# Kernel tuning notes

Measured on AMD Instinct MI355X. Metric: run time of the kernel, lower is better.

The kernel has to match this reference:

```python
import jax, jax.numpy as jnp
import numpy as np

T = 5          # Newton-Schulz iterations
EPS = 1e-5
NC = 64        # num_channels per group

def setup_inputs() -> dict:
    key = jax.random.key(0)
    X = jax.random.normal(key, (128, 256, 32, 32), dtype=jnp.float32)
    weight = jnp.ones((1, 256, 1, 1), dtype=jnp.float32)
    bias = jnp.zeros((1, 256, 1, 1), dtype=jnp.float32)
    return {"X": X, "weight": weight, "bias": bias}

def _iternorm(X):
    B, C, H, W = X.shape
    g = C // NC
    # [B,C,H,W] -> [C,B,H,W] -> [g, nc, m]
    x = jnp.transpose(X, (1, 0, 2, 3)).reshape(g, NC, -1)
    m = x.shape[-1]
    mean = x.mean(-1, keepdims=True)
    xc = x - mean                                   # [g, nc, m]
    I = jnp.eye(NC, dtype=X.dtype)
    Sigma = EPS * I + jnp.einsum('gdm,gem->gde', xc, xc) / m
    # rTr = 1 / trace(Sigma) per group
    rTr = 1.0 / jnp.trace(Sigma, axis1=1, axis2=2)[:, None, None]
    Sn = Sigma * rTr                                # normalized covariance
    P = jnp.broadcast_to(I, (g, NC, NC))
    for _ in range(T):
        P3 = jnp.matmul(jnp.matmul(P, P), P)
        P = 1.5 * P - 0.5 * jnp.matmul(P3, Sn)
    wm = P * jnp.sqrt(rTr)                          # whitening matrix [g,nc,nc]
    xn = jnp.matmul(wm, xc)                         # [g, nc, m]
    Xn = jnp.transpose(xn.reshape(C, B, H, W), (1, 0, 2, 3))
    return Xn

def reference(X, weight, bias):
    Xn = _iternorm(X)
    return Xn * weight + bias
```

## Files before the change

### kernel.cpp

```cpp
#include <hip/hip_runtime.h>
#include <hip/hip_bf16.h>
#include <cstddef>
#include <cstdint>

typedef __attribute__((ext_vector_type(8))) short s16x8;
typedef __attribute__((ext_vector_type(4))) float f32x4;

namespace {
constexpr int NB   = 128;
constexpr int NCH  = 256;
constexpr int SPA  = 1024;
constexpr int NCC  = 64;
constexpr int MT   = NB * SPA;
constexpr float EPSV = 1e-5f;
}

__device__ inline unsigned short f2bf(float f) {
    union { float f; unsigned u; } v; v.f = f;
    unsigned r = v.u + 0x7fffu + ((v.u >> 16) & 1u);
    return (unsigned short)(r >> 16);
}

__device__ inline s16x8 cvt8(float4 a, float4 b) {
    union { __hip_bfloat162 h[4]; s16x8 s; } u;
    u.h[0] = __float22bfloat162_rn(make_float2(a.x, a.y));
    u.h[1] = __float22bfloat162_rn(make_float2(a.z, a.w));
    u.h[2] = __float22bfloat162_rn(make_float2(b.x, b.y));
    u.h[3] = __float22bfloat162_rn(make_float2(b.z, b.w));
    return u.s;
}

__device__ inline s16x8 pack8(const float* v) {
    union { __hip_bfloat162 h[4]; s16x8 s; } u;
    u.h[0] = __float22bfloat162_rn(make_float2(v[0], v[1]));
    u.h[1] = __float22bfloat162_rn(make_float2(v[2], v[3]));
    u.h[2] = __float22bfloat162_rn(make_float2(v[4], v[5]));
    u.h[3] = __float22bfloat162_rn(make_float2(v[6], v[7]));
    return u.s;
}

__device__ inline void issue8(const float* const base[4], int ks, float4 r[4][2]) {
#pragma unroll
    for (int cb = 0; cb < 4; ++cb) {
        r[cb][0] = *reinterpret_cast<const float4*>(base[cb] + ks * 32);
        r[cb][1] = *reinterpret_cast<const float4*>(base[cb] + ks * 32 + 4);
    }
}
__device__ inline void finish8(const float4 r[4][2], s16x8 frag[4], float csum[4]) {
#pragma unroll
    for (int cb = 0; cb < 4; ++cb) {
        const float4 f0 = r[cb][0], f1 = r[cb][1];
        csum[cb] += (f0.x + f0.y) + (f0.z + f0.w) + (f1.x + f1.y) + (f1.z + f1.w);
        frag[cb] = cvt8(f0, f1);
    }
}
__device__ inline void mfma10(const s16x8 frag[4], f32x4 acc[10]) {
    int n = 0;
#pragma unroll
    for (int i = 0; i < 4; ++i)
#pragma unroll
        for (int j = i; j < 4; ++j) {
            acc[n] = __builtin_amdgcn_mfma_f32_16x16x32_bf16(frag[i], frag[j], acc[n], 0, 0, 0);
            ++n;
        }
}

__global__ __launch_bounds__(256) void zca_stats(const float* __restrict__ X,
                                                 float* __restrict__ Gpart,
                                                 float* __restrict__ Spart) {
    const int bid = blockIdx.x;
    const int g = bid >> 7, b = bid & 127;
    const int t = threadIdx.x;
    const int w = t >> 6, l = t & 63;
    const int lr = l & 15, gq = l >> 4;

    const float* xs = X + ((size_t)b * NCH + (size_t)g * NCC) * SPA;

    const float* base[4];
#pragma unroll
    for (int cb = 0; cb < 4; ++cb)
        base[cb] = xs + (size_t)(cb * 16 + lr) * SPA + w * 256 + gq * 8;

    f32x4 acc[10];
#pragma unroll
    for (int n = 0; n < 10; ++n) acc[n] = (f32x4){0.f, 0.f, 0.f, 0.f};
    float csum[4] = {0.f, 0.f, 0.f, 0.f};

    float4 rA[4][2], rB[4][2];
    issue8(base, 0, rA);
    issue8(base, 1, rB);
#pragma unroll
    for (int ks = 0; ks < 8; ks += 2) {
        s16x8 frag[4];
        finish8(rA, frag, csum);
        if (ks + 2 < 8) issue8(base, ks + 2, rA);
        mfma10(frag, acc);
        finish8(rB, frag, csum);
        if (ks + 3 < 8) issue8(base, ks + 3, rB);
        mfma10(frag, acc);
    }

    __shared__ float Gl[64 * 67];
    __shared__ float Ssl[4][64];

#pragma unroll
    for (int cb = 0; cb < 4; ++cb) {
        float s = csum[cb];
        s += __shfl_xor(s, 16, 64);
        s += __shfl_xor(s, 32, 64);
        if (gq == 0) Ssl[w][cb * 16 + lr] = s;
    }

    for (int ph = 0; ph < 4; ++ph) {
        if (w == ph) {
            int n = 0;
#pragma unroll
            for (int i = 0; i < 4; ++i)
#pragma unroll
                for (int j = i; j < 4; ++j) {
#pragma unroll
                    for (int q = 0; q < 4; ++q) {
                        const int d = i * 16 + gq * 4 + q;
                        const int e = j * 16 + lr;
                        const float val = acc[n][q];
                        if (ph == 0) {
                            Gl[d * 67 + e] = val;
                            if (i != j) Gl[e * 67 + d] = val;
                        } else {
                            Gl[d * 67 + e] += val;
                            if (i != j) Gl[e * 67 + d] += val;
                        }
                    }
                    ++n;
                }
        }
        __syncthreads();
    }

#pragma unroll
    for (int i = 0; i < 16; ++i) {
        const int idx = i * 256 + t;
        const int d = idx >> 6, e = idx & 63;
        Gpart[(size_t)bid * 4096 + idx] = Gl[d * 67 + e];
    }
    if (t < 64)
        Spart[(size_t)bid * 64 + t] =
            ((Ssl[0][t] + Ssl[1][t]) + (Ssl[2][t] + Ssl[3][t]));
}

__global__ __launch_bounds__(256) void zca_reduce(const float* __restrict__ Gpart,
                                                  const float* __restrict__ Spart,
                                                  float* __restrict__ Gsum,
                                                  float* __restrict__ Ssub) {
    const int g = blockIdx.x >> 4, eb = blockIdx.x & 15;
    const int t = threadIdx.x;
    const float* p = Gpart + (size_t)g * 128 * 4096 + eb * 256 + t;
    float a0 = 0.f, a1 = 0.f, a2 = 0.f, a3 = 0.f;
    for (int q = 0; q < 128; q += 4) {
        a0 += p[(size_t)(q + 0) * 4096];
        a1 += p[(size_t)(q + 1) * 4096];
        a2 += p[(size_t)(q + 2) * 4096];
        a3 += p[(size_t)(q + 3) * 4096];
    }
    Gsum[(size_t)g * 4096 + eb * 256 + t] = (a0 + a1) + (a2 + a3);

    if (t < 64) {
        float s = 0.f;
        for (int q = 0; q < 8; ++q)
            s += Spart[(size_t)(g * 128 + eb * 8 + q) * 64 + t];
        Ssub[(size_t)(g * 16 + eb) * 64 + t] = s;
    }
}

__global__ __launch_bounds__(256) void zca_newton(const float* __restrict__ Gsum,
                                                  const float* __restrict__ Ssub,
                                                  const float* __restrict__ weight,
                                                  const float* __restrict__ bias,
                                                  short* __restrict__ wmB,
                                                  float* __restrict__ betaOut) {
    const int g = blockIdx.x;
    const int t = threadIdx.x;
    const int v = t >> 4;
    const int u = t & 15;

    __shared__ float Pm[64 * 65];
    __shared__ float Sn[64 * 65];
    __shared__ float Ta[64 * 65];
    __shared__ float meanS[64];
    __shared__ float scal[2];

    if (t < 64) {
        float s = 0.f;
        for (int eb = 0; eb < 16; ++eb) s += Ssub[(size_t)(g * 16 + eb) * 64 + t];
        meanS[t] = s * (1.0f / MT);
    }
    __syncthreads();

#pragma unroll
    for (int i = 0; i < 16; ++i) {
        int idx = i * 256 + t;
        int d = idx >> 6, e = idx & 63;
        float sig = Gsum[(size_t)g * 4096 + idx] * (1.0f / MT)
                    - meanS[d] * meanS[e] + (d == e ? EPSV : 0.f);
        Sn[d * 65 + e] = sig;
    }
    __syncthreads();

    if (t < 64) {
        float tr = Sn[t * 65 + t];
        for (int off = 32; off > 0; off >>= 1) tr += __shfl_down(tr, off, 64);
        if (t == 0) {
            scal[0] = 1.0f / tr;
            scal[1] = sqrtf(1.0f / tr);
        }
    }
    __syncthreads();
    const float rTr = scal[0];

#pragma unroll
    for (int i = 0; i < 16; ++i) {
        int idx = i * 256 + t;
        int d = idx >> 6, e = idx & 63;
        Sn[d * 65 + e] *= rTr;
        Pm[d * 65 + e] = (d == e) ? 1.f : 0.f;
    }
    __syncthreads();

    auto mm = [&](const float* A, const float* Bm, float* r) {
#pragma unroll
        for (int q = 0; q < 16; ++q) r[q] = 0.f;
        for (int k = 0; k < 64; ++k) {
            float a[4], bb[4];
#pragma unroll
            for (int i = 0; i < 4; ++i) a[i] = A[(v + 16 * i) * 65 + k];
#pragma unroll
            for (int j = 0; j < 4; ++j) bb[j] = Bm[k * 65 + (u + 16 * j)];
#pragma unroll
            for (int i = 0; i < 4; ++i)
#pragma unroll
                for (int j = 0; j < 4; ++j) r[i * 4 + j] += a[i] * bb[j];
        }
    };
    auto storeTa = [&](const float* r) {
#pragma unroll
        for (int q = 0; q < 16; ++q)
            Ta[(v + 16 * (q >> 2)) * 65 + (u + 16 * (q & 3))] = r[q];
    };

    for (int it = 0; it < 5; ++it) {
        float r[16];
        mm(Pm, Sn, r);
        storeTa(r);
        __syncthreads();
        mm(Pm, Ta, r);
        __syncthreads();
        storeTa(r);
        __syncthreads();
        mm(Pm, Ta, r);
        __syncthreads();
#pragma unroll
        for (int q = 0; q < 16; ++q) {
            int rr = v + 16 * (q >> 2);
            int cc = u + 16 * (q & 3);
            Pm[rr * 65 + cc] = 1.5f * Pm[rr * 65 + cc] - 0.5f * r[q];
        }
        __syncthreads();
    }

    const float srTr = scal[1];
#pragma unroll
    for (int i = 0; i < 16; ++i) {
        int idx = i * 256 + t;
        int d = idx >> 6, e = idx & 63;
        float wv = weight[g * NCC + d];
        wmB[(size_t)g * 4096 + d * 64 + e] = (short)f2bf(Pm[d * 65 + e] * srTr * wv);
    }
    if (t < 64) {
        int d = t;
        float s = 0.f;
        for (int e = 0; e < 64; ++e) s += Pm[d * 65 + e] * meanS[e];
        betaOut[g * NCC + d] = bias[g * NCC + d] - weight[g * NCC + d] * srTr * s;
    }
}

__global__ __launch_bounds__(256) void zca_apply(const float* __restrict__ X,
                                                 const short* __restrict__ wmB,
                                                 const float* __restrict__ beta,
                                                 float* __restrict__ out) {
    const int bid = blockIdx.x;
    const int g  = bid & 3;
    const int qm = (bid >> 2) & 3;
    const int b  = bid >> 4;
    const int t  = threadIdx.x;
    const int w  = t >> 6, l = t & 63;
    const int lr = l & 15, gq = l >> 4;

    __shared__ float Xt[64][64];
    __shared__ float Ot[64][64];

    s16x8 wa[4][2];
#pragma unroll
    for (int i = 0; i < 4; ++i)
#pragma unroll
        for (int kc = 0; kc < 2; ++kc)
            wa[i][kc] = *reinterpret_cast<const s16x8*>(
                wmB + (size_t)g * 4096 + (16 * i + lr) * 64 + kc * 32 + gq * 8);

    const int ch = t >> 4, s4 = t & 15;
    float bst[4];
#pragma unroll
    for (int i = 0; i < 4; ++i) bst[i] = beta[g * NCC + i * 16 + ch];

    const float* xb = X + ((size_t)b * NCH + (size_t)g * NCC) * SPA + qm * 256;
    float* ob = out + ((size_t)b * NCH + (size_t)g * NCC) * SPA + qm * 256;

    const int lh = l >> 4;

    for (int tile = 0; tile < 4; ++tile) {
#pragma unroll
        for (int i = 0; i < 4; ++i) {
            const float* gsrc = xb + (size_t)(i * 16 + w * 4 + lh) * SPA
                                + tile * 64 + (l & 15) * 4;
            __builtin_amdgcn_global_load_lds(
                (const __attribute__((address_space(1))) void*)gsrc,
                (__attribute__((address_space(3))) void*)&Xt[i * 16 + w * 4][0],
                16, 0, 0);
        }
        asm volatile("s_waitcnt vmcnt(0)" ::: "memory");
        __syncthreads();

        float v[2][8];
#pragma unroll
        for (int kc = 0; kc < 2; ++kc)
#pragma unroll
            for (int j = 0; j < 8; ++j)
                v[kc][j] = Xt[kc * 32 + gq * 8 + j][w * 16 + lr];

        s16x8 bf0 = pack8(v[0]);
        s16x8 bf1 = pack8(v[1]);

        f32x4 acc[4];
#pragma unroll
        for (int i = 0; i < 4; ++i) acc[i] = (f32x4){0.f, 0.f, 0.f, 0.f};
#pragma unroll
        for (int i = 0; i < 4; ++i) {
            acc[i] = __builtin_amdgcn_mfma_f32_16x16x32_bf16(wa[i][0], bf0, acc[i], 0, 0, 0);
            acc[i] = __builtin_amdgcn_mfma_f32_16x16x32_bf16(wa[i][1], bf1, acc[i], 0, 0, 0);
        }

#pragma unroll
        for (int i = 0; i < 4; ++i)
#pragma unroll
            for (int q = 0; q < 4; ++q)
                Ot[16 * i + 4 * gq + q][w * 16 + lr] = acc[i][q];
        __syncthreads();

#pragma unroll
        for (int i = 0; i < 4; ++i) {
            float4 o = *reinterpret_cast<const float4*>(&Ot[i * 16 + ch][s4 * 4]);
            o.x += bst[i]; o.y += bst[i]; o.z += bst[i]; o.w += bst[i];
            *reinterpret_cast<float4*>(
                ob + (size_t)(i * 16 + ch) * SPA + tile * 64 + s4 * 4) = o;
        }
    }
}

extern "C" void kernel_launch(void* const* d_in, const int* in_sizes, int n_in,
                              void* d_out, int out_size, void* d_ws, size_t ws_size,
                              hipStream_t stream) {
    const float* X      = (const float*)d_in[0];
    const float* weight = (const float*)d_in[1];
    const float* bias   = (const float*)d_in[2];
    float* out = (float*)d_out;

    float* ws    = (float*)d_ws;
    float* Gpart = ws;
    float* Spart = Gpart + (size_t)512 * 4096;
    float* Gsum  = Spart + (size_t)512 * 64;
    float* Ssub  = Gsum + (size_t)4 * 4096;
    float* betaW = Ssub + (size_t)4 * 16 * 64;
    short* wmB   = (short*)(betaW + 256);

    zca_stats <<<dim3(512),  dim3(256), 0, stream>>>(X, Gpart, Spart);
    zca_reduce<<<dim3(64),   dim3(256), 0, stream>>>(Gpart, Spart, Gsum, Ssub);
    zca_newton<<<dim3(4),    dim3(256), 0, stream>>>(Gsum, Ssub, weight, bias, wmB, betaW);
    zca_apply <<<dim3(2048), dim3(256), 0, stream>>>(X, wmB, betaW, out);
}
```

Baseline: 138.8 us.

## Split zca_stats blocks in half along spatial dim to double grid parallelism

Each stats block now handles half of a (group, batch) spatial extent, so the grid doubles from 512 to 1024 blocks and each wave does 4 k-steps instead of 8. The load pipeline is reorganised into two half-channel register sets per step. The goal is better occupancy and latency hiding across the CUs for this bandwidth-bound Gram pass. In exchange, the partial-Gram workspace doubles, and zca_reduce must sum 256 partials per group instead of 128, which adds memory traffic in that small kernel.

```diff
diff --git a/kernel.cpp b/kernel.cpp
--- a/kernel.cpp
+++ b/kernel.cpp
@@ -39,19 +39,20 @@
     return u.s;
 }
 
-__device__ inline void issue8(const float* const base[4], int ks, float4 r[4][2]) {
-#pragma unroll
-    for (int cb = 0; cb < 4; ++cb) {
-        r[cb][0] = *reinterpret_cast<const float4*>(base[cb] + ks * 32);
-        r[cb][1] = *reinterpret_cast<const float4*>(base[cb] + ks * 32 + 4);
-    }
-}
-__device__ inline void finish8(const float4 r[4][2], s16x8 frag[4], float csum[4]) {
-#pragma unroll
-    for (int cb = 0; cb < 4; ++cb) {
-        const float4 f0 = r[cb][0], f1 = r[cb][1];
-        csum[cb] += (f0.x + f0.y) + (f0.z + f0.w) + (f1.x + f1.y) + (f1.z + f1.w);
-        frag[cb] = cvt8(f0, f1);
+__device__ inline void issue4(const float* const base[4], int ks, int p, float4 r[2][2]) {
+#pragma unroll
+    for (int c = 0; c < 2; ++c) {
+        const float* q = base[p * 2 + c] + ks * 32;
+        r[c][0] = *reinterpret_cast<const float4*>(q);
+        r[c][1] = *reinterpret_cast<const float4*>(q + 4);
+    }
+}
+__device__ inline void finish4(const float4 r[2][2], s16x8* frag2, float* cs2) {
+#pragma unroll
+    for (int c = 0; c < 2; ++c) {
+        const float4 f0 = r[c][0], f1 = r[c][1];
+        cs2[c] += (f0.x + f0.y) + (f0.z + f0.w) + (f1.x + f1.y) + (f1.z + f1.w);
+        frag2[c] = cvt8(f0, f1);
     }
 }
 __device__ inline void mfma10(const s16x8 frag[4], f32x4 acc[10]) {
@@ -69,7 +70,7 @@
                                                  float* __restrict__ Gpart,
                                                  float* __restrict__ Spart) {
     const int bid = blockIdx.x;
-    const int g = bid >> 7, b = bid & 127;
+    const int g = bid >> 8, b = (bid >> 1) & 127, half = bid & 1;
     const int t = threadIdx.x;
     const int w = t >> 6, l = t & 63;
     const int lr = l & 15, gq = l >> 4;
@@ -79,24 +80,23 @@
     const float* base[4];
 #pragma unroll
     for (int cb = 0; cb < 4; ++cb)
-        base[cb] = xs + (size_t)(cb * 16 + lr) * SPA + w * 256 + gq * 8;
+        base[cb] = xs + (size_t)(cb * 16 + lr) * SPA + half * 512 + w * 128 + gq * 8;
 
     f32x4 acc[10];
 #pragma unroll
     for (int n = 0; n < 10; ++n) acc[n] = (f32x4){0.f, 0.f, 0.f, 0.f};
     float csum[4] = {0.f, 0.f, 0.f, 0.f};
 
-    float4 rA[4][2], rB[4][2];
-    issue8(base, 0, rA);
-    issue8(base, 1, rB);
-#pragma unroll
-    for (int ks = 0; ks < 8; ks += 2) {
-        s16x8 frag[4];
-        finish8(rA, frag, csum);
-        if (ks + 2 < 8) issue8(base, ks + 2, rA);
-        mfma10(frag, acc);
-        finish8(rB, frag, csum);
-        if (ks + 3 < 8) issue8(base, ks + 3, rB);
+    float4 rA[2][2], rB[2][2];
+    s16x8 frag[4];
+    issue4(base, 0, 0, rA);
+    issue4(base, 0, 1, rB);
+#pragma unroll
+    for (int ks = 0; ks < 4; ++ks) {
+        finish4(rA, &frag[0], &csum[0]);
+        if (ks + 1 < 4) issue4(base, ks + 1, 0, rA);
+        finish4(rB, &frag[2], &csum[2]);
+        if (ks + 1 < 4) issue4(base, ks + 1, 1, rB);
         mfma10(frag, acc);
     }
 
@@ -154,9 +154,9 @@
                                                   float* __restrict__ Ssub) {
     const int g = blockIdx.x >> 4, eb = blockIdx.x & 15;
     const int t = threadIdx.x;
-    const float* p = Gpart + (size_t)g * 128 * 4096 + eb * 256 + t;
+    const float* p = Gpart + (size_t)g * 256 * 4096 + eb * 256 + t;
     float a0 = 0.f, a1 = 0.f, a2 = 0.f, a3 = 0.f;
-    for (int q = 0; q < 128; q += 4) {
+    for (int q = 0; q < 256; q += 4) {
         a0 += p[(size_t)(q + 0) * 4096];
         a1 += p[(size_t)(q + 1) * 4096];
         a2 += p[(size_t)(q + 2) * 4096];
@@ -166,8 +166,8 @@
 
     if (t < 64) {
         float s = 0.f;
-        for (int q = 0; q < 8; ++q)
-            s += Spart[(size_t)(g * 128 + eb * 8 + q) * 64 + t];
+        for (int q = 0; q < 16; ++q)
+            s += Spart[(size_t)(g * 256 + eb * 16 + q) * 64 + t];
         Ssub[(size_t)(g * 16 + eb) * 64 + t] = s;
     }
 }
@@ -375,13 +375,13 @@
 
     float* ws    = (float*)d_ws;
     float* Gpart = ws;
-    float* Spart = Gpart + (size_t)512 * 4096;
-    float* Gsum  = Spart + (size_t)512 * 64;
+    float* Spart = Gpart + (size_t)1024 * 4096;
+    float* Gsum  = Spart + (size_t)1024 * 64;
     float* Ssub  = Gsum + (size_t)4 * 4096;
     float* betaW = Ssub + (size_t)4 * 16 * 64;
     short* wmB   = (short*)(betaW + 256);
 
-    zca_stats <<<dim3(512),  dim3(256), 0, stream>>>(X, Gpart, Spart);
+    zca_stats <<<dim3(1024), dim3(256), 0, stream>>>(X, Gpart, Spart);
     zca_reduce<<<dim3(64),   dim3(256), 0, stream>>>(Gpart, Spart, Gsum, Ssub);
     zca_newton<<<dim3(4),    dim3(256), 0, stream>>>(Gsum, Ssub, weight, bias, wmB, betaW);
     zca_apply <<<dim3(2048), dim3(256), 0, stream>>>(X, wmB, betaW, out);
```

Result: slower. 153.9 us (+10.9%).
